# Kernel tuning notes

Measured on AMD Instinct MI355X. Metric: run time of the kernel, lower is better.

## Reference

```python
import jax, jax.numpy as jnp
import numpy as np

N = 100000      # nodes
E = 1600000     # edges (before self loops)
D_IN, D_H, D_OUT = 128, 64, 32
EPS = 1e-5      # BatchNorm eps
SLOPE = 0.2     # GATConv leaky_relu negative slope


def setup_inputs() -> dict:
    key = jax.random.key(0)
    ks = jax.random.split(key, 32)
    def lin(k, fi, fo):
        return (jax.random.normal(k, (fi, fo), jnp.float32) / np.float32(np.sqrt(fi)))
    def vec(k, d):
        return jax.random.normal(k, (d,), jnp.float32) * 0.1
    inp = {
        "x": jax.random.normal(ks[0], (N, D_IN), jnp.float32),
        "edge_index": jax.random.randint(ks[1], (2, E), 0, N, jnp.int32),
        # layer 1: GATConv(in->h) + BN(h)
        "W1": lin(ks[2], D_IN, D_H), "as1": vec(ks[3], D_H), "ad1": vec(ks[4], D_H), "b1": jnp.zeros((D_H,), jnp.float32),
        "g1": jnp.ones((D_H,), jnp.float32), "be1": jnp.zeros((D_H,), jnp.float32),
        "rm1": vec(ks[5], D_H), "rv1": jax.random.uniform(ks[6], (D_H,), jnp.float32) + 0.5,
        # layer 2: GATConv(h->h) + BN(h)
        "W2": lin(ks[7], D_H, D_H), "as2": vec(ks[8], D_H), "ad2": vec(ks[9], D_H), "b2": jnp.zeros((D_H,), jnp.float32),
        "g2": jnp.ones((D_H,), jnp.float32), "be2": jnp.zeros((D_H,), jnp.float32),
        "rm2": vec(ks[10], D_H), "rv2": jax.random.uniform(ks[11], (D_H,), jnp.float32) + 0.5,
        # layer 3: GATConv(h->out)
        "W3": lin(ks[12], D_H, D_OUT), "as3": vec(ks[13], D_OUT), "ad3": vec(ks[14], D_OUT), "b3": jnp.zeros((D_OUT,), jnp.float32),
    }
    return inp


def _gat_conv(x, W, a_s, a_d, b, src, dst):
    # PyG GATConv, heads=1: gather -> leaky_relu score -> segment softmax over dst -> scatter-add
    h = x @ W                                             # [N, F]
    e = jax.nn.leaky_relu((h @ a_s)[src] + (h @ a_d)[dst], SLOPE)   # [E']
    m = jax.ops.segment_max(e, dst, num_segments=N)       # stable softmax per destination
    p = jnp.exp(e - m[dst])
    s = jax.ops.segment_sum(p, dst, num_segments=N)
    alpha = p / s[dst]                                    # [E']
    out = jax.ops.segment_sum(h[src] * alpha[:, None], dst, num_segments=N)
    return out + b


def _bn(x, g, b, rm, rv):
    # BatchNorm1d in eval mode (running stats)
    return (x - rm) * jax.lax.rsqrt(rv + EPS) * g + b


def reference(x, edge_index, W1, as1, ad1, b1, g1, be1, rm1, rv1,
              W2, as2, ad2, b2, g2, be2, rm2, rv2, W3, as3, ad3, b3):
    # add self loops (GATConv default add_self_loops=True)
    loop = jnp.arange(N, dtype=edge_index.dtype)
    src = jnp.concatenate([edge_index[0], loop])
    dst = jnp.concatenate([edge_index[1], loop])
    h = _gat_conv(x, W1, as1, ad1, b1, src, dst)
    h = jax.nn.relu(_bn(h, g1, be1, rm1, rv1))            # dropout is identity in eval
    h = _gat_conv(h, W2, as2, ad2, b2, src, dst)
    h = jax.nn.relu(_bn(h, g2, be2, rm2, rv2))
    return _gat_conv(h, W3, as3, ad3, b3, src, dst)
```

## Files before the change

kernel.cpp:

```cpp
#include <hip/hip_runtime.h>


#define D_IN 128
#define EPS 1e-5f
#define SLOPE 0.2f

template <int K, int F>
__global__ __launch_bounds__(256) void gemm_scores(
    const float* __restrict__ X, const float* __restrict__ W,
    const float* __restrict__ a_s, const float* __restrict__ a_d,
    float* __restrict__ H, float* __restrict__ HS, float* __restrict__ HD,
    int n)
{
    constexpr int XS  = (K == 128) ? K : (K + 4);
    constexpr int CPT = F / 16;
    __shared__ float Xs[64 * XS];
    __shared__ float Ws[K * F];

    const int tid  = threadIdx.x;
    const int row0 = blockIdx.x * 64;

    for (int i = tid * 4; i < 64 * K; i += 256 * 4) {
        int row = i / K, col = i % K;
        float4 v = make_float4(0.f, 0.f, 0.f, 0.f);
        if (row0 + row < n)
            v = *(const float4*)&X[(size_t)(row0 + row) * K + col];
        *(float4*)&Xs[row * XS + col] = v;
    }
    for (int i = tid; i < K * F / 4; i += 256)
        *(float4*)&Ws[i * 4] = ((const float4*)W)[i];
    __syncthreads();

    const int tr = tid >> 4, tc = tid & 15;
    float acc[4][CPT];
    #pragma unroll
    for (int i = 0; i < 4; i++)
        #pragma unroll
        for (int j = 0; j < CPT; j++) acc[i][j] = 0.f;

    for (int k = 0; k < K; k += 4) {
        float xv[4][4];
        #pragma unroll
        for (int i = 0; i < 4; i++) {
            float4 t = *(const float4*)&Xs[(tr + 16 * i) * XS + k];
            xv[i][0] = t.x; xv[i][1] = t.y; xv[i][2] = t.z; xv[i][3] = t.w;
        }
        #pragma unroll
        for (int kk = 0; kk < 4; kk++) {
            float wv[CPT];
            if constexpr (CPT == 4) {
                float4 t = *(const float4*)&Ws[(k + kk) * F + tc * 4];
                wv[0] = t.x; wv[1] = t.y; wv[2] = t.z; wv[3] = t.w;
            } else {
                float2 t = *(const float2*)&Ws[(k + kk) * F + tc * 2];
                wv[0] = t.x; wv[1] = t.y;
            }
            #pragma unroll
            for (int i = 0; i < 4; i++)
                #pragma unroll
                for (int j = 0; j < CPT; j++)
                    acc[i][j] += xv[i][kk] * wv[j];
        }
    }

    float cs[CPT], cd[CPT];
    #pragma unroll
    for (int j = 0; j < CPT; j++) {
        cs[j] = a_s[tc * CPT + j];
        cd[j] = a_d[tc * CPT + j];
    }
    #pragma unroll
    for (int i = 0; i < 4; i++) {
        int row = row0 + tr + 16 * i;
        float vs = 0.f, vd = 0.f;
        #pragma unroll
        for (int j = 0; j < CPT; j++) { vs += acc[i][j] * cs[j]; vd += acc[i][j] * cd[j]; }
        #pragma unroll
        for (int m = 1; m < 16; m <<= 1) {
            vs += __shfl_xor(vs, m, 64);
            vd += __shfl_xor(vd, m, 64);
        }
        if (row < n) {
            if constexpr (CPT == 4) {
                float4 t = make_float4(acc[i][0], acc[i][1], acc[i][2], acc[i][3]);
                *(float4*)&H[(size_t)row * F + tc * 4] = t;
            } else {
                float2 t = make_float2(acc[i][0], acc[i][1]);
                *(float2*)&H[(size_t)row * F + tc * 2] = t;
            }
            if (tc == 0) { HS[row] = vs; HD[row] = vd; }
        }
    }
}

__global__ __launch_bounds__(256) void hist_kernel(
    const int* __restrict__ dst, int* __restrict__ deg, int E)
{
    int e4 = (blockIdx.x * 256 + threadIdx.x) * 4;
    if (e4 + 3 < E) {
        int4 d4 = *(const int4*)&dst[e4];
        atomicAdd(&deg[d4.x], 1);
        atomicAdd(&deg[d4.y], 1);
        atomicAdd(&deg[d4.z], 1);
        atomicAdd(&deg[d4.w], 1);
    } else {
        for (int e = e4; e < E; ++e) atomicAdd(&deg[dst[e]], 1);
    }
}

__global__ __launch_bounds__(512) void scan_phase1(
    const int* __restrict__ deg, int* __restrict__ rowptr,
    int* __restrict__ sums, int n)
{
    __shared__ int s[512];
    int t = threadIdx.x;
    int i = blockIdx.x * 512 + t;
    int v = (i < n) ? deg[i] : 0;
    s[t] = v;
    __syncthreads();
    for (int off = 1; off < 512; off <<= 1) {
        int x = (t >= off) ? s[t - off] : 0;
        __syncthreads();
        s[t] += x;
        __syncthreads();
    }
    if (i < n) rowptr[i] = s[t] - v;
    if (t == 511) sums[blockIdx.x] = s[511];
}

__global__ __launch_bounds__(512) void scan_phase2(int* __restrict__ sums, int nb)
{
    __shared__ int s[512];
    int t = threadIdx.x;
    int v = (t < nb) ? sums[t] : 0;
    s[t] = v;
    __syncthreads();
    for (int off = 1; off < 512; off <<= 1) {
        int x = (t >= off) ? s[t - off] : 0;
        __syncthreads();
        s[t] += x;
        __syncthreads();
    }
    if (t < nb) sums[t] = s[t] - v;
}

__global__ __launch_bounds__(256) void scan_phase3(
    int* __restrict__ rowptr, const int* __restrict__ sums, int n, int E)
{
    int i = blockIdx.x * 256 + threadIdx.x;
    if (i < n) rowptr[i] += sums[i >> 9];
    else if (i == n) rowptr[n] = E;
}

__global__ __launch_bounds__(256) void scatter_kernel(
    const int* __restrict__ src, const int* __restrict__ dst,
    int* __restrict__ rowptr ,
    int* __restrict__ esrc, int E)
{
    int e4 = (blockIdx.x * 256 + threadIdx.x) * 4;
    if (e4 + 3 < E) {
        int4 s4 = *(const int4*)&src[e4];
        int4 d4 = *(const int4*)&dst[e4];
        esrc[atomicAdd(&rowptr[d4.x], 1)] = s4.x;
        esrc[atomicAdd(&rowptr[d4.y], 1)] = s4.y;
        esrc[atomicAdd(&rowptr[d4.z], 1)] = s4.z;
        esrc[atomicAdd(&rowptr[d4.w], 1)] = s4.w;
    } else {
        for (int e = e4; e < E; ++e)
            esrc[atomicAdd(&rowptr[dst[e]], 1)] = src[e];
    }
}

template <int F, bool BN>
__global__ __launch_bounds__(256) void gat_aggregate(
    const int* __restrict__ rowptr, const int* __restrict__ esrc,
    const float* __restrict__ H, const float* __restrict__ HS,
    const float* __restrict__ HD,
    const float* __restrict__ b, const float* __restrict__ g,
    const float* __restrict__ be, const float* __restrict__ rm,
    const float* __restrict__ rv,
    float* __restrict__ OUT, int n)
{
    int t = blockIdx.x * 256 + threadIdx.x;
    int node = t / F, f = t % F;
    if (node >= n) return;

    float hd = HD[node];
    float sc = HS[node] + hd;
    sc = sc > 0.f ? sc : SLOPE * sc;
    float p = __expf(sc);
    float s = p;
    float acc = p * H[(size_t)node * F + f];

    const int beg = node ? rowptr[node - 1] : 0;
    const int end = rowptr[node];
    int j = beg;
    const int len = end - beg;

    const int end8 = beg + (len & ~7);
    for (; j < end8; j += 8) {
        int   sr[8];
        float a[8], h[8];
        #pragma unroll
        for (int u = 0; u < 8; ++u) sr[u] = esrc[j + u];
        #pragma unroll
        for (int u = 0; u < 8; ++u) a[u] = HS[sr[u]];
        #pragma unroll
        for (int u = 0; u < 8; ++u) h[u] = H[(size_t)sr[u] * F + f];
        #pragma unroll
        for (int u = 0; u < 8; ++u) {
            float e2 = a[u] + hd;
            e2 = e2 > 0.f ? e2 : SLOPE * e2;
            float p2 = __expf(e2);
            s   += p2;
            acc += p2 * h[u];
        }
    }
    if (len & 4) {
        int   sr[4];
        float a[4], h[4];
        #pragma unroll
        for (int u = 0; u < 4; ++u) sr[u] = esrc[j + u];
        #pragma unroll
        for (int u = 0; u < 4; ++u) a[u] = HS[sr[u]];
        #pragma unroll
        for (int u = 0; u < 4; ++u) h[u] = H[(size_t)sr[u] * F + f];
        #pragma unroll
        for (int u = 0; u < 4; ++u) {
            float e2 = a[u] + hd;
            e2 = e2 > 0.f ? e2 : SLOPE * e2;
            float p2 = __expf(e2);
            s   += p2;
            acc += p2 * h[u];
        }
        j += 4;
    }
    for (; j < end; ++j) {
        int sr = esrc[j];
        float e2 = HS[sr] + hd;
        e2 = e2 > 0.f ? e2 : SLOPE * e2;
        float p2 = __expf(e2);
        s += p2;
        acc += p2 * H[(size_t)sr * F + f];
    }

    float v = acc / s + b[f];
    if constexpr (BN) {
        v = (v - rm[f]) * rsqrtf(rv[f] + EPS) * g[f] + be[f];
        v = v > 0.f ? v : 0.f;
    }
    OUT[(size_t)node * F + f] = v;
}

extern "C" void kernel_launch(void* const* d_in, const int* in_sizes, int n_in,
                              void* d_out, int out_size, void* d_ws, size_t ws_size,
                              hipStream_t stream)
{
    const float* x   = (const float*)d_in[0];
    const int*   ei  = (const int*)d_in[1];
    const float* W1  = (const float*)d_in[2];
    const float* as1 = (const float*)d_in[3];
    const float* ad1 = (const float*)d_in[4];
    const float* b1  = (const float*)d_in[5];
    const float* g1  = (const float*)d_in[6];
    const float* be1 = (const float*)d_in[7];
    const float* rm1 = (const float*)d_in[8];
    const float* rv1 = (const float*)d_in[9];
    const float* W2  = (const float*)d_in[10];
    const float* as2 = (const float*)d_in[11];
    const float* ad2 = (const float*)d_in[12];
    const float* b2  = (const float*)d_in[13];
    const float* g2  = (const float*)d_in[14];
    const float* be2 = (const float*)d_in[15];
    const float* rm2 = (const float*)d_in[16];
    const float* rv2 = (const float*)d_in[17];
    const float* W3  = (const float*)d_in[18];
    const float* as3 = (const float*)d_in[19];
    const float* ad3 = (const float*)d_in[20];
    const float* b3  = (const float*)d_in[21];

    const int n  = in_sizes[0] / D_IN;
    const int E  = in_sizes[1] / 2;
    const int* src = ei;
    const int* dst = ei + E;

    float* ws = (float*)d_ws;
    float* H      = ws;
    float* X2     = H  + (size_t)n * 64;
    float* HS     = X2 + (size_t)n * 64;
    float* HD     = HS + n;
    int*   deg    = (int*)(HD + n);
    int*   rowptr = deg + n;
    int*   sums   = rowptr + (n + 1);
    int*   esrc   = sums + 512;

    const int NB = (n + 511) / 512;
    const int e4_grid = (E / 4 + 255) / 256;

    hipMemsetAsync(deg, 0, (size_t)n * 4, stream);
    hist_kernel<<<e4_grid, 256, 0, stream>>>(dst, deg, E);
    scan_phase1<<<NB, 512, 0, stream>>>(deg, rowptr, sums, n);
    scan_phase2<<<1, 512, 0, stream>>>(sums, NB);
    scan_phase3<<<(n + 256) / 256, 256, 0, stream>>>(rowptr, sums, n, E);
    scatter_kernel<<<e4_grid, 256, 0, stream>>>(src, dst, rowptr, esrc, E);

    const int gemm_grid = (n + 63) / 64;
    const int ag64_grid = (int)(((size_t)n * 64 + 255) / 256);
    const int ag32_grid = (int)(((size_t)n * 32 + 255) / 256);

    gemm_scores<128, 64><<<gemm_grid, 256, 0, stream>>>(x, W1, as1, ad1, H, HS, HD, n);
    gat_aggregate<64, true><<<ag64_grid, 256, 0, stream>>>(
        rowptr, esrc, H, HS, HD, b1, g1, be1, rm1, rv1, X2, n);

    gemm_scores<64, 64><<<gemm_grid, 256, 0, stream>>>(X2, W2, as2, ad2, H, HS, HD, n);
    gat_aggregate<64, true><<<ag64_grid, 256, 0, stream>>>(
        rowptr, esrc, H, HS, HD, b2, g2, be2, rm2, rv2, X2, n);

    gemm_scores<64, 32><<<gemm_grid, 256, 0, stream>>>(X2, W3, as3, ad3, H, HS, HD, n);
    gat_aggregate<32, false><<<ag32_grid, 256, 0, stream>>>(
        rowptr, esrc, H, HS, HD, b3, nullptr, nullptr, nullptr, nullptr,
        (float*)d_out, n);
}
```

Baseline: 587.1 us.

## Replace atomic CSR scatter with two-pass bucketed binning and shared-memory scatter

After: 503.1 us. -14.3%, faster.

```diff
diff --git a/kernel.cpp b/kernel.cpp
--- a/kernel.cpp
+++ b/kernel.cpp
@@ -152,22 +152,118 @@
     else if (i == n) rowptr[n] = E;
 }
 
-__global__ __launch_bounds__(256) void scatter_kernel(
+__global__ __launch_bounds__(256) void bcur_init(
+    const int* __restrict__ rowptr, int* __restrict__ bcur, int n, int B)
+{
+    int b = blockIdx.x * 256 + threadIdx.x;
+    if (b < B) {
+        int nb = b << 9;
+        if (nb > n) nb = n;
+        bcur[b] = rowptr[nb];
+    }
+}
+
+#define CHUNK 4096
+#define NBKT  256
+
+__global__ __launch_bounds__(256) void bin_kernel(
     const int* __restrict__ src, const int* __restrict__ dst,
-    int* __restrict__ rowptr ,
-    int* __restrict__ esrc, int E)
-{
-    int e4 = (blockIdx.x * 256 + threadIdx.x) * 4;
-    if (e4 + 3 < E) {
-        int4 s4 = *(const int4*)&src[e4];
-        int4 d4 = *(const int4*)&dst[e4];
-        esrc[atomicAdd(&rowptr[d4.x], 1)] = s4.x;
-        esrc[atomicAdd(&rowptr[d4.y], 1)] = s4.y;
-        esrc[atomicAdd(&rowptr[d4.z], 1)] = s4.z;
-        esrc[atomicAdd(&rowptr[d4.w], 1)] = s4.w;
+    int* __restrict__ bcur, int* __restrict__ binned, int E)
+{
+    __shared__ int2 stage[CHUNK];
+    __shared__ int cnt[NBKT], loff[NBKT], lcur[NBKT], shift[NBKT];
+
+    const int tid  = threadIdx.x;
+    const int base = blockIdx.x * CHUNK;
+    const int ccnt = min(CHUNK, E - base);
+
+    if (tid < NBKT) { cnt[tid] = 0; }
+    __syncthreads();
+
+    int es[16], ed[16];
+    const int tb = base + tid * 16;
+    const int tm = max(0, min(16, E - tb));
+    #pragma unroll 4
+    for (int k = 0; k < 16; ++k) {
+        if (k < tm) {
+            es[k] = src[tb + k];
+            ed[k] = dst[tb + k];
+            atomicAdd(&cnt[ed[k] >> 9], 1);
+        }
+    }
+    __syncthreads();
+
+    loff[tid] = cnt[tid];
+    __syncthreads();
+    for (int off = 1; off < NBKT; off <<= 1) {
+        int x = (tid >= off) ? loff[tid - off] : 0;
+        __syncthreads();
+        loff[tid] += x;
+        __syncthreads();
+    }
+    int excl = loff[tid] - cnt[tid];
+    __syncthreads();
+    loff[tid] = excl;
+    lcur[tid] = 0;
+    if (cnt[tid] > 0) {
+        int g = atomicAdd(&bcur[tid], cnt[tid]);
+        shift[tid] = g - excl;
+    }
+    __syncthreads();
+
+    #pragma unroll 4
+    for (int k = 0; k < 16; ++k) {
+        if (k < tm) {
+            int b = ed[k] >> 9;
+            int pos = loff[b] + atomicAdd(&lcur[b], 1);
+            stage[pos] = make_int2(((ed[k] & 511) << 17) | es[k], b);
+        }
+    }
+    __syncthreads();
+
+    for (int i = tid; i < ccnt; i += 256) {
+        int2 v = stage[i];
+        binned[shift[v.y] + i] = v.x;
+    }
+}
+
+#define CAP 12288
+
+__global__ __launch_bounds__(256) void bucket_scatter(
+    const int* __restrict__ rowptr, const int* __restrict__ binned,
+    int* __restrict__ esrc, int n)
+{
+    __shared__ int outbuf[CAP];
+    __shared__ int cur[512];
+
+    const int tid  = threadIdx.x;
+    const int b    = blockIdx.x;
+    const int nb   = b << 9;
+    const int ne   = min(n, nb + 512);
+    const int nn   = ne - nb;
+    const int sbeg = rowptr[nb];
+    const int send = rowptr[ne];
+    const int cnt  = send - sbeg;
+
+    for (int l = tid; l < nn; l += 256)
+        cur[l] = rowptr[nb + l] - sbeg;
+    __syncthreads();
+
+    if (cnt <= CAP) {
+        for (int i = sbeg + tid; i < send; i += 256) {
+            int v = binned[i];
+            int slot = atomicAdd(&cur[v >> 17], 1);
+            outbuf[slot] = v & 0x1FFFF;
+        }
+        __syncthreads();
+        for (int i = tid; i < cnt; i += 256)
+            esrc[sbeg + i] = outbuf[i];
     } else {
-        for (int e = e4; e < E; ++e)
-            esrc[atomicAdd(&rowptr[dst[e]], 1)] = src[e];
+        for (int i = sbeg + tid; i < send; i += 256) {
+            int v = binned[i];
+            int slot = atomicAdd(&cur[v >> 17], 1);
+            esrc[sbeg + slot] = v & 0x1FFFF;
+        }
     }
 }
 
@@ -192,8 +288,8 @@
     float s = p;
     float acc = p * H[(size_t)node * F + f];
 
-    const int beg = node ? rowptr[node - 1] : 0;
-    const int end = rowptr[node];
+    const int beg = rowptr[node];
+    const int end = rowptr[node + 1];
     int j = beg;
     const int len = end - beg;
 
@@ -283,6 +379,7 @@
     const int E  = in_sizes[1] / 2;
     const int* src = ei;
     const int* dst = ei + E;
+    const int B  = (n + 511) >> 9;
 
     float* ws = (float*)d_ws;
     float* H      = ws;
@@ -293,16 +390,19 @@
     int*   rowptr = deg + n;
     int*   sums   = rowptr + (n + 1);
     int*   esrc   = sums + 512;
+    int*   bcur   = esrc + E;
+    int*   binned = (int*)X2;
 
     const int NB = (n + 511) / 512;
-    const int e4_grid = (E / 4 + 255) / 256;
 
     hipMemsetAsync(deg, 0, (size_t)n * 4, stream);
-    hist_kernel<<<e4_grid, 256, 0, stream>>>(dst, deg, E);
+    hist_kernel<<<(E / 4 + 255) / 256, 256, 0, stream>>>(dst, deg, E);
     scan_phase1<<<NB, 512, 0, stream>>>(deg, rowptr, sums, n);
     scan_phase2<<<1, 512, 0, stream>>>(sums, NB);
     scan_phase3<<<(n + 256) / 256, 256, 0, stream>>>(rowptr, sums, n, E);
-    scatter_kernel<<<e4_grid, 256, 0, stream>>>(src, dst, rowptr, esrc, E);
+    bcur_init<<<1, 256, 0, stream>>>(rowptr, bcur, n, B);
+    bin_kernel<<<(E + CHUNK - 1) / CHUNK, 256, 0, stream>>>(src, dst, bcur, binned, E);
+    bucket_scatter<<<B, 256, 0, stream>>>(rowptr, binned, esrc, n);
 
     const int gemm_grid = (n + 63) / 64;
     const int ag64_grid = (int)(((size_t)n * 64 + 255) / 256);
```
